# Performance work log

Measured on AMD Instinct MI355X. Metric: run time of the kernel, lower is better.

The kernel has to match this reference:

```python
import jax, jax.numpy as jnp
import numpy as np

# Layer configuration (from init_kwargs)
T = 32
TSEQ = jnp.linspace(1.0 / T, 1.0, T, dtype=jnp.float32)  # tseq grid
N_HOM_DIMS = 2      # dimensions = [0, 1]
KMAX = 4            # KK = [0,1,2,3] -> top-4 landscapes

B, N, P = 128, 256 * 256, 4096  # batch, grid cells, persistence pairs


def setup_inputs() -> dict:
    key = jax.random.key(0)
    k1, k2, k3, k4 = jax.random.split(key, 4)
    fun_value = jax.random.uniform(k1, (B, N), dtype=jnp.float32)
    birth_idx = jax.random.randint(k2, (B, P), 0, N, dtype=jnp.int32)
    death_idx = jax.random.randint(k3, (B, P), 0, N, dtype=jnp.int32)
    pair_dim = jax.random.randint(k4, (B, P), 0, N_HOM_DIMS, dtype=jnp.int32)
    return {"fun_value": fun_value, "birth_idx": birth_idx,
            "death_idx": death_idx, "pair_dim": pair_dim}


def reference(fun_value, birth_idx, death_idx, pair_dim):
    # Gather birth/death filtration values of each persistence pair
    # (this is fun_value[locationBirth] / fun_value[locationDeath]).
    b = jnp.take_along_axis(fun_value, birth_idx, axis=-1)   # [B, P]
    d = jnp.take_along_axis(fun_value, death_idx, axis=-1)   # [B, P]
    # Tent functions: fab[b, t, p] = max(min(tseq[t] - birth_p, death_p - tseq[t]), 0)
    fab = jnp.maximum(
        jnp.minimum(TSEQ[None, :, None] - b[:, None, :],
                    d[:, None, :] - TSEQ[None, :, None]),
        0.0)                                                  # [B, T, P]
    # Restrict pairs to each homology dimension; out-of-dim pairs become the
    # zero padding the original code uses in its fab buffer.
    dims = jnp.arange(N_HOM_DIMS, dtype=pair_dim.dtype)
    in_dim = pair_dim[:, None, None, :] == dims[None, :, None, None]  # [B, D, 1, P]
    fab_d = jnp.where(in_dim, fab[:, None, :, :], 0.0)        # [B, D, T, P]
    # Landscape = top-KMAX values over pairs (== -sort(-fab)[..., KK]).
    land, _ = jax.lax.top_k(fab_d, KMAX)                      # [B, D, T, KMAX]
    return land
```

## Files before the change

kernel.cpp:

```cpp
#include <hip/hip_runtime.h>

#define B_ 128
#define N_ 65536
#define P_ 4096
#define T_ 32
#define D_ 2
#define K_ 4
#define S_ 8
#define PPB 512

#define INS(v0, v1, v2, v3, val)                                  \
    {                                                             \
        float _x = fminf(v0, val); v0 = fmaxf(v0, val);           \
        float _y = fminf(v1, _x);  v1 = fmaxf(v1, _x);            \
        float _z = fminf(v2, _y);  v2 = fmaxf(v2, _y);            \
        v3 = fmaxf(v3, _z);                                       \
    }

__global__ __launch_bounds__(256) void fused_scan(
        const float* __restrict__ fun,
        const int* __restrict__ bidx,
        const int* __restrict__ didx,
        const int* __restrict__ pdim,
        float* __restrict__ partial) {
    __shared__ __align__(16) float2 bdS[PPB + 8];
    __shared__ int cnt0S[8];
    __shared__ int cnt1S[8];
    __shared__ float mrg[4][64][4];

    int bid   = blockIdx.x;
    int xcd   = bid & 7;
    int seq   = bid >> 3;
    int batch = xcd * 16 + (seq & 15);
    int slice = seq >> 4;

    int tid  = threadIdx.x;
    int lane = tid & 63;
    int wave = tid >> 6;
    int base = batch * P_ + slice * PPB;

    const float* f = fun + (size_t)batch * N_;
    int2 bi = ((const int2*)(bidx + base))[tid];
    int2 di = ((const int2*)(didx + base))[tid];
    int2 pd = ((const int2*)(pdim + base))[tid];
    float be = f[bi.x], de = f[di.x];
    float bo = f[bi.y], dd = f[di.y];

    bool k0e = (pd.x == 0) && (de > be);
    bool k1e = (pd.x == 1) && (de > be);
    bool k0o = (pd.y == 0) && (dd > bo);
    bool k1o = (pd.y == 1) && (dd > bo);

    unsigned long long b0e = __ballot(k0e), b1e = __ballot(k1e);
    unsigned long long b0o = __ballot(k0o), b1o = __ballot(k1o);
    if (lane == 0) {
        cnt0S[wave * 2]     = __popcll(b0e);
        cnt0S[wave * 2 + 1] = __popcll(b0o);
        cnt1S[wave * 2]     = __popcll(b1e);
        cnt1S[wave * 2 + 1] = __popcll(b1o);
    }
    __syncthreads();

    int ce = wave * 2, co = ce + 1;
    int pre0e = 0, pre0o = 0, pre1e = 0, pre1o = 0, tot0 = 0, tot1 = 0;
    #pragma unroll
    for (int c = 0; c < 8; ++c) {
        int c0 = cnt0S[c], c1 = cnt1S[c];
        if (c < ce) { pre0e += c0; pre1e += c1; }
        if (c < co) { pre0o += c0; pre1o += c1; }
        tot0 += c0; tot1 += c1;
    }
    int A  = (tot0 + 3) & ~3;
    int L1 = (tot1 + 3) & ~3;

    unsigned long long lm = (1ull << lane) - 1ull;
    if (k0e) bdS[pre0e + __popcll(b0e & lm)]     = make_float2(be, de);
    if (k1e) bdS[A + pre1e + __popcll(b1e & lm)] = make_float2(be, de);
    if (k0o) bdS[pre0o + __popcll(b0o & lm)]     = make_float2(bo, dd);
    if (k1o) bdS[A + pre1o + __popcll(b1o & lm)] = make_float2(bo, dd);
    if (tid < A - tot0)                    bdS[tot0 + tid]           = make_float2(4.f, -4.f);
    if (tid >= 4 && tid - 4 < L1 - tot1)   bdS[A + tot1 + (tid - 4)] = make_float2(4.f, -4.f);
    __syncthreads();

    int half = lane >> 5;
    int t    = lane & 31;
    float tf = (float)(t + 1) * 0.03125f;

    float a0 = 0.f, a1 = 0.f, a2 = 0.f, a3 = 0.f;
    float c0 = 0.f, c1 = 0.f, c2 = 0.f, c3 = 0.f;

    const float2* bd0 = bdS + 2 * half;
    #pragma unroll 2
    for (int j = wave * 4; j < A; j += 16) {
        float4 q = *(const float4*)(bd0 + j);
        float v0 = fminf(tf - q.x, q.y - tf);
        float v1 = fminf(tf - q.z, q.w - tf);
        INS(a0, a1, a2, a3, v0);
        INS(a0, a1, a2, a3, v1);
    }
    #pragma unroll 2
    for (int j = wave * 4; j < L1; j += 16) {
        float4 q = *(const float4*)(bd0 + A + j);
        float v0 = fminf(tf - q.x, q.y - tf);
        float v1 = fminf(tf - q.z, q.w - tf);
        INS(c0, c1, c2, c3, v0);
        INS(c0, c1, c2, c3, v1);
    }

    float u0 = (half == 0) ? a0 : c0, w0 = (half == 0) ? c0 : a0;
    float u1 = (half == 0) ? a1 : c1, w1 = (half == 0) ? c1 : a1;
    float u2 = (half == 0) ? a2 : c2, w2 = (half == 0) ? c2 : a2;
    float u3 = (half == 0) ? a3 : c3, w3 = (half == 0) ? c3 : a3;
    float q;
    q = __shfl_xor(w0, 32); INS(u0, u1, u2, u3, q);
    q = __shfl_xor(w1, 32); INS(u0, u1, u2, u3, q);
    q = __shfl_xor(w2, 32); INS(u0, u1, u2, u3, q);
    q = __shfl_xor(w3, 32); INS(u0, u1, u2, u3, q);

    mrg[wave][lane][0] = u0;
    mrg[wave][lane][1] = u1;
    mrg[wave][lane][2] = u2;
    mrg[wave][lane][3] = u3;
    __syncthreads();

    if (wave == 0) {
        float v0 = 0.f, v1 = 0.f, v2 = 0.f, v3 = 0.f;
        #pragma unroll
        for (int w = 0; w < 4; ++w) {
            #pragma unroll
            for (int k = 0; k < 4; ++k) {
                float val = mrg[w][lane][k];
                INS(v0, v1, v2, v3, val);
            }
        }
        ((float4*)partial)[((size_t)batch * S_ + slice) * 64 + lane] =
            make_float4(v0, v1, v2, v3);
    }
}

__global__ __launch_bounds__(256) void final_merge(
        const float* __restrict__ partial,
        float* __restrict__ out) {
    int tid   = blockIdx.x * 256 + threadIdx.x;
    int batch = tid >> 6;
    int combo = tid & 63;
    const float4* src = (const float4*)partial + (size_t)batch * S_ * 64 + combo;
    float v0 = 0.f, v1 = 0.f, v2 = 0.f, v3 = 0.f;
    #pragma unroll
    for (int s = 0; s < S_; ++s) {
        float4 p = src[(size_t)s * 64];
        INS(v0, v1, v2, v3, p.x);
        INS(v0, v1, v2, v3, p.y);
        INS(v0, v1, v2, v3, p.z);
        INS(v0, v1, v2, v3, p.w);
    }
    ((float4*)out)[tid] = make_float4(v0, v1, v2, v3);
}

extern "C" void kernel_launch(void* const* d_in, const int* in_sizes, int n_in,
                              void* d_out, int out_size, void* d_ws, size_t ws_size,
                              hipStream_t stream) {
    const float* fun  = (const float*)d_in[0];
    const int*   bidx = (const int*)d_in[1];
    const int*   didx = (const int*)d_in[2];
    const int*   pdim = (const int*)d_in[3];
    float* out = (float*)d_out;

    float* partial = (float*)d_ws;

    fused_scan<<<B_ * S_, 256, 0, stream>>>(fun, bidx, didx, pdim, partial);
    final_merge<<<(B_ * 64) / 256, 256, 0, stream>>>(partial, out);
}
```

Baseline: 87.73 us.

## Stream each batch's fun_value chunk to warm cache and split pairs finer

Each block now reads a contiguous 4096-float chunk of its batch's fun_value row with coalesced float4 loads. An empty asm statement keeps those loads alive, so the row is pulled into the shared L2 of the XCD where all slices of that batch run. The goal is for the random birth and death gathers from sibling blocks to hit cache rather than issue scattered DRAM line fetches. The pair split also doubles from 8 to 16 slices of 256 pairs, giving one pair per thread, and adds an occupancy hint of 8 blocks per SM. The cost is a full extra sequential read of fun_value plus twice as many partials for the final merge.

Result: no change. 89.10 us (+1.6%).

```diff
diff --git a/kernel.cpp b/kernel.cpp
--- a/kernel.cpp
+++ b/kernel.cpp
@@ -6,8 +6,9 @@
 #define T_ 32
 #define D_ 2
 #define K_ 4
-#define S_ 8
-#define PPB 512
+#define S_ 16
+#define PPB 256
+#define CHUNK (N_ / S_)
 
 #define INS(v0, v1, v2, v3, val)                                  \
     {                                                             \
@@ -17,16 +18,16 @@
         v3 = fmaxf(v3, _z);                                       \
     }
 
-__global__ __launch_bounds__(256) void fused_scan(
+__global__ __launch_bounds__(256, 8) void fused_scan(
         const float* __restrict__ fun,
         const int* __restrict__ bidx,
         const int* __restrict__ didx,
         const int* __restrict__ pdim,
         float* __restrict__ partial) {
     __shared__ __align__(16) float2 bdS[PPB + 8];
-    __shared__ int cnt0S[8];
-    __shared__ int cnt1S[8];
-    __shared__ float mrg[4][64][4];
+    __shared__ int cnt0S[4];
+    __shared__ int cnt1S[4];
+    __shared__ __align__(16) float4 mrg[4][64];
 
     int bid   = blockIdx.x;
     int xcd   = bid & 7;
@@ -37,49 +38,52 @@
     int tid  = threadIdx.x;
     int lane = tid & 63;
     int wave = tid >> 6;
-    int base = batch * P_ + slice * PPB;
 
     const float* f = fun + (size_t)batch * N_;
-    int2 bi = ((const int2*)(bidx + base))[tid];
-    int2 di = ((const int2*)(didx + base))[tid];
-    int2 pd = ((const int2*)(pdim + base))[tid];
-    float be = f[bi.x], de = f[di.x];
-    float bo = f[bi.y], dd = f[di.y];
+    int p = batch * P_ + slice * PPB + tid;
 
-    bool k0e = (pd.x == 0) && (de > be);
-    bool k1e = (pd.x == 1) && (de > be);
-    bool k0o = (pd.y == 0) && (dd > bo);
-    bool k1o = (pd.y == 1) && (dd > bo);
+    int bi = bidx[p];
+    int di = didx[p];
+    int pd = pdim[p];
 
-    unsigned long long b0e = __ballot(k0e), b1e = __ballot(k1e);
-    unsigned long long b0o = __ballot(k0o), b1o = __ballot(k1o);
+    const float4* pf = (const float4*)(f + slice * CHUNK);
+    float4 w0 = pf[tid];
+    float4 w1 = pf[tid + 256];
+    float4 w2 = pf[tid + 512];
+    float4 w3 = pf[tid + 768];
+
+    float b = f[bi], d = f[di];
+
+    bool k0 = (d > b) && (pd == 0);
+    bool k1 = (d > b) && (pd == 1);
+    unsigned long long bal0 = __ballot(k0);
+    unsigned long long bal1 = __ballot(k1);
     if (lane == 0) {
-        cnt0S[wave * 2]     = __popcll(b0e);
-        cnt0S[wave * 2 + 1] = __popcll(b0o);
-        cnt1S[wave * 2]     = __popcll(b1e);
-        cnt1S[wave * 2 + 1] = __popcll(b1o);
+        cnt0S[wave] = __popcll(bal0);
+        cnt1S[wave] = __popcll(bal1);
     }
+
+    float ka = (w0.x + w0.y + w0.z + w0.w) + (w1.x + w1.y + w1.z + w1.w)
+             + (w2.x + w2.y + w2.z + w2.w) + (w3.x + w3.y + w3.z + w3.w);
+    asm volatile("" :: "v"(ka));
+
     __syncthreads();
 
-    int ce = wave * 2, co = ce + 1;
-    int pre0e = 0, pre0o = 0, pre1e = 0, pre1o = 0, tot0 = 0, tot1 = 0;
+    int pre0 = 0, pre1 = 0, tot0 = 0, tot1 = 0;
     #pragma unroll
-    for (int c = 0; c < 8; ++c) {
+    for (int c = 0; c < 4; ++c) {
         int c0 = cnt0S[c], c1 = cnt1S[c];
-        if (c < ce) { pre0e += c0; pre1e += c1; }
-        if (c < co) { pre0o += c0; pre1o += c1; }
+        if (c < wave) { pre0 += c0; pre1 += c1; }
         tot0 += c0; tot1 += c1;
     }
     int A  = (tot0 + 3) & ~3;
     int L1 = (tot1 + 3) & ~3;
 
     unsigned long long lm = (1ull << lane) - 1ull;
-    if (k0e) bdS[pre0e + __popcll(b0e & lm)]     = make_float2(be, de);
-    if (k1e) bdS[A + pre1e + __popcll(b1e & lm)] = make_float2(be, de);
-    if (k0o) bdS[pre0o + __popcll(b0o & lm)]     = make_float2(bo, dd);
-    if (k1o) bdS[A + pre1o + __popcll(b1o & lm)] = make_float2(bo, dd);
-    if (tid < A - tot0)                    bdS[tot0 + tid]           = make_float2(4.f, -4.f);
-    if (tid >= 4 && tid - 4 < L1 - tot1)   bdS[A + tot1 + (tid - 4)] = make_float2(4.f, -4.f);
+    if (k0) bdS[pre0 + __popcll(bal0 & lm)]     = make_float2(b, d);
+    if (k1) bdS[A + pre1 + __popcll(bal1 & lm)] = make_float2(b, d);
+    if (tid < A - tot0)                  bdS[tot0 + tid]           = make_float2(4.f, -4.f);
+    if (tid >= 4 && tid - 4 < L1 - tot1) bdS[A + tot1 + (tid - 4)] = make_float2(4.f, -4.f);
     __syncthreads();
 
     int half = lane >> 5;
@@ -107,31 +111,28 @@
         INS(c0, c1, c2, c3, v1);
     }
 
-    float u0 = (half == 0) ? a0 : c0, w0 = (half == 0) ? c0 : a0;
-    float u1 = (half == 0) ? a1 : c1, w1 = (half == 0) ? c1 : a1;
-    float u2 = (half == 0) ? a2 : c2, w2 = (half == 0) ? c2 : a2;
-    float u3 = (half == 0) ? a3 : c3, w3 = (half == 0) ? c3 : a3;
+    float u0 = (half == 0) ? a0 : c0, x0 = (half == 0) ? c0 : a0;
+    float u1 = (half == 0) ? a1 : c1, x1 = (half == 0) ? c1 : a1;
+    float u2 = (half == 0) ? a2 : c2, x2 = (half == 0) ? c2 : a2;
+    float u3 = (half == 0) ? a3 : c3, x3 = (half == 0) ? c3 : a3;
     float q;
-    q = __shfl_xor(w0, 32); INS(u0, u1, u2, u3, q);
-    q = __shfl_xor(w1, 32); INS(u0, u1, u2, u3, q);
-    q = __shfl_xor(w2, 32); INS(u0, u1, u2, u3, q);
-    q = __shfl_xor(w3, 32); INS(u0, u1, u2, u3, q);
+    q = __shfl_xor(x0, 32); INS(u0, u1, u2, u3, q);
+    q = __shfl_xor(x1, 32); INS(u0, u1, u2, u3, q);
+    q = __shfl_xor(x2, 32); INS(u0, u1, u2, u3, q);
+    q = __shfl_xor(x3, 32); INS(u0, u1, u2, u3, q);
 
-    mrg[wave][lane][0] = u0;
-    mrg[wave][lane][1] = u1;
-    mrg[wave][lane][2] = u2;
-    mrg[wave][lane][3] = u3;
+    mrg[wave][lane] = make_float4(u0, u1, u2, u3);
     __syncthreads();
 
     if (wave == 0) {
         float v0 = 0.f, v1 = 0.f, v2 = 0.f, v3 = 0.f;
         #pragma unroll
         for (int w = 0; w < 4; ++w) {
-            #pragma unroll
-            for (int k = 0; k < 4; ++k) {
-                float val = mrg[w][lane][k];
-                INS(v0, v1, v2, v3, val);
-            }
+            float4 m = mrg[w][lane];
+            INS(v0, v1, v2, v3, m.x);
+            INS(v0, v1, v2, v3, m.y);
+            INS(v0, v1, v2, v3, m.z);
+            INS(v0, v1, v2, v3, m.w);
         }
         ((float4*)partial)[((size_t)batch * S_ + slice) * 64 + lane] =
             make_float4(v0, v1, v2, v3);
```
